# Optimization experiments

Hardware: AMD Instinct MI355X
Metric: run time of the kernel (lower is better)

## Reference

```python
import jax, jax.numpy as jnp
from jax import lax
import numpy as np

# pywt Wavelet('db4') decomposition filters
DEC_LO = jnp.array([-0.010597401784997278, 0.032883011666982945, 0.030841381835986965,
                    -0.18703481171888114, -0.027983769416983848, 0.6308807679295904,
                    0.7148465705525415, 0.23037781330885523], dtype=jnp.float32)
DEC_HI = jnp.array([-0.23037781330885523, 0.7148465705525415, -0.6308807679295904,
                    -0.027983769416983848, 0.18703481171888114, 0.030841381835986965,
                    -0.032883011666982945, -0.010597401784997278], dtype=jnp.float32)
FLT = 8
BN_INV = np.float32(1.0 / np.sqrt(1.0 + 1e-5))  # BatchNorm eval: running_mean=0, running_var=1


def dwt_db4(v):
    """Vectorized pywt.dwt(v, 'db4', mode='symmetric') along the last axis.
    v: (..., n) -> (cA, cD), each (..., (n+FLT-1)//2).
    pywt: symmetric-pad by FLT-1, true convolution with filter, take valid[1::2].
    Equivalent: correlate padded[1:...] with flipped filter, stride 2."""
    n = v.shape[-1]
    out_len = (n + FLT - 1) // 2
    xp = jnp.pad(v, [(0, 0)] * (v.ndim - 1) + [(FLT - 1, FLT - 1)], mode='symmetric')
    xp = xp[..., 1:1 + 2 * (out_len - 1) + FLT]
    lead = v.shape[:-1]
    xr = xp.reshape(-1, 1, xp.shape[-1])                      # (N*, 1, L)
    kern = jnp.stack([DEC_LO[::-1], DEC_HI[::-1]])[:, None, :]  # (2, 1, 8)
    y = lax.conv_general_dilated(xr, kern, (2,), 'VALID',
                                 dimension_numbers=('NCH', 'OIH', 'NCH'))
    return y[:, 0].reshape(lead + (out_len,)), y[:, 1].reshape(lead + (out_len,))


def conv_bn_relu(x, w, g, b):
    # x: (B, C, S); w: (O, I, K) no bias; BN in eval mode; ReLU; dropout off (eval)
    k = w.shape[-1]
    p = (k - 1) // 2
    y = lax.conv_general_dilated(x, w, (1,), [(p, p)],
                                 dimension_numbers=('NCH', 'OIH', 'NCH'))
    return jax.nn.relu((g * BN_INV)[None, :, None] * y + b[None, :, None])


def setup_inputs() -> dict:
    key = jax.random.key(0)
    ks = jax.random.split(key, 16)
    C, S, B = 88, 2048, 4
    d = dict()
    d['x'] = jax.random.normal(ks[0], (B, S, C), dtype=jnp.float32)
    d['w1'] = jax.random.normal(ks[1], (C, C, 1), dtype=jnp.float32) * 0.05
    d['w2a'] = jax.random.normal(ks[2], (C, C, 1), dtype=jnp.float32) * 0.05
    d['w2b'] = jax.random.normal(ks[3], (C, C, 3), dtype=jnp.float32) * 0.05
    d['w3a'] = jax.random.normal(ks[4], (C, C, 1), dtype=jnp.float32) * 0.05
    d['w3b'] = jax.random.normal(ks[5], (C, C, 3), dtype=jnp.float32) * 0.05
    d['w3c'] = jax.random.normal(ks[6], (C, C, 5), dtype=jnp.float32) * 0.05
    for nm in ['g1', 'g2a', 'g2b', 'g3a', 'g3b', 'g3c']:
        d[nm] = jnp.ones((C,), dtype=jnp.float32)
    for nm in ['b1', 'b2a', 'b2b', 'b3a', 'b3b', 'b3c']:
        d[nm] = jnp.zeros((C,), dtype=jnp.float32)
    d['Wmp'] = jax.random.normal(ks[7], (C, 3 * C), dtype=jnp.float32) * 0.05
    d['bmp'] = jnp.zeros((C,), dtype=jnp.float32)
    d['Wq'] = jax.random.normal(ks[8], (C, C), dtype=jnp.float32) * 0.1
    d['Wk'] = jax.random.normal(ks[9], (C, C), dtype=jnp.float32) * 0.1
    d['Wv'] = jax.random.normal(ks[10], (C, C), dtype=jnp.float32) * 0.1
    d['Wout'] = jax.random.normal(ks[11], (C, 112), dtype=jnp.float32) * 0.05
    d['bout'] = jnp.zeros((C,), dtype=jnp.float32)
    return d


def reference(x, w1, g1, b1, w2a, g2a, b2a, w2b, g2b, b2b,
              w3a, g3a, b3a, w3b, g3b, b3b, w3c, g3c, b3c,
              Wmp, bmp, Wq, Wk, Wv, Wout, bout):
    B, S, H = x.shape
    head = 4
    dk = H // head                                # 22
    wd = dk // 2 + 3 if dk % 2 == 0 else (dk + 1) // 2 + 3  # 14
    xt = jnp.swapaxes(x, 1, 2)                    # (B, C, S)
    # mutil_Parallel: three conv lines + fuse + residual
    x1 = conv_bn_relu(xt, w1, g1, b1)
    x2 = conv_bn_relu(conv_bn_relu(xt, w2a, g2a, b2a), w2b, g2b, b2b)
    x3 = conv_bn_relu(conv_bn_relu(conv_bn_relu(xt, w3a, g3a, b3a), w3b, g3b, b3b), w3c, g3c, b3c)
    cat = jnp.concatenate([x1, x2, x3], axis=1)   # (B, 3C, S)
    mp = jnp.einsum('bcs,oc->bso', cat, Wmp) + bmp + x  # (B, S, C)
    identity = mp
    # multi-head attention with wavelet-transformed values
    scale = dk ** (-0.5)
    q = jnp.einsum('bsh,oh->bso', mp, Wq).reshape(B, S, head, dk).transpose(0, 2, 1, 3) * scale
    k = jnp.einsum('bsh,oh->bso', mp, Wk).reshape(B, S, head, dk).transpose(0, 2, 1, 3)
    v = jnp.einsum('bsh,oh->bso', mp, Wv).reshape(B, S, head, dk).transpose(0, 2, 1, 3)
    attn = jax.nn.softmax(jnp.einsum('bhqd,bhkd->bhqk', q, k), axis=-1)  # (B,4,S,S)
    cA, cD = dwt_db4(v)                           # each (B, 4, S, 14)
    wcd = jnp.einsum('bhqk,bhkd->bhqd', attn, cD)  # (B, 4, S, 14)
    xo = jax.nn.relu(wcd.transpose(0, 2, 1, 3).reshape(B, S, head * wd))
    cAr = cA.reshape(B, S, head * wd)             # faithful to source's direct .view
    out = jnp.concatenate([xo, cAr], axis=-1) @ Wout.T + bout
    return identity + out
```

## Files before the change

### kernel.cpp

```cpp
#include <hip/hip_runtime.h>

#define BN_INV  0.99999500003749981f
#define QSCALE  0.21320071635561041f

typedef unsigned int uint;
typedef unsigned short u16;
typedef __attribute__((ext_vector_type(8))) short s16x8;
typedef __attribute__((ext_vector_type(4))) float f32x4;

#define OFF_BCAT 0
#define OFF_V    512
#define OFF_MP   721408
#define SW0    2884608
#define SB1    (SW0)
#define SB2B   (SW0+30720)
#define SB3B   (SW0+67584)
#define SB3C   (SW0+104448)
#define SBMP   (SW0+165888)
#define SBQKV  (SW0+202752)
#define SBOUT  (SW0+239616)
#define SXB    3148800
#define SXCAT  3869696
#define SX2    6032384
#define ST3B   6753280
#define SX3    7474176
#define SMPB   8195072
#define SQB    3869696
#define SKB    4918272
#define SCDT   5966848
#define SXOB   6753280

__constant__ float c_dlo[8] = {-0.010597401784997278f, 0.032883011666982945f,
    0.030841381835986965f, -0.18703481171888114f, -0.02798376941698385f,
    0.6308807679295904f, 0.7148465705525415f, 0.23037781330885523f};
__constant__ float c_dhi[8] = {-0.23037781330885523f, 0.7148465705525415f,
    -0.6308807679295904f, -0.02798376941698385f, 0.18703481171888114f,
    0.030841381835986965f, -0.032883011666982945f, -0.010597401784997278f};

__device__ __forceinline__ u16 f2bf(float f) {
    uint u = __float_as_uint(f);
    uint r = u + 0x7fffu + ((u >> 16) & 1u);
    return (u16)(r >> 16);
}

__global__ __launch_bounds__(256) void prepk(
    const float* __restrict__ x,
    const float* __restrict__ w1, const float* __restrict__ w2a, const float* __restrict__ w2b,
    const float* __restrict__ w3a, const float* __restrict__ w3b, const float* __restrict__ w3c,
    const float* __restrict__ g1, const float* __restrict__ g2a, const float* __restrict__ g2b,
    const float* __restrict__ g3a, const float* __restrict__ g3b, const float* __restrict__ g3c,
    const float* __restrict__ b1, const float* __restrict__ b2a, const float* __restrict__ b3a,
    const float* __restrict__ Wmp, const float* __restrict__ Wq, const float* __restrict__ Wk,
    const float* __restrict__ Wv, const float* __restrict__ Wout, float* __restrict__ ws)
{
    u16* wu = (u16*)ws;
    int r = blockIdx.x * 256 + threadIdx.x;
    if (r < 264) {
        ws[OFF_BCAT + r] = (r < 88) ? b1[r] : (r < 176 ? b2a[r-88] : b3a[r-176]);
        return;
    }
    r -= 264;
    if (r < 320*96) {
        int n = r / 96, kk = r % 96; float v = 0.f;
        if (kk < 88 && n < 264) {
            if (n < 88)       v = w1 [n*88+kk]       * g1 [n];
            else if (n < 176) v = w2a[(n-88)*88+kk]  * g2a[n-88];
            else              v = w3a[(n-176)*88+kk] * g3a[n-176];
            v *= BN_INV;
        }
        wu[SB1 + r] = f2bf(v); return;
    }
    r -= 320*96;
    if (r < 128*288) {
        int n = r / 288, kk = r % 288, t = kk/96, i = kk%96; float v = 0.f;
        if (n < 88 && i < 88) v = w2b[n*264 + i*3 + t] * g2b[n] * BN_INV;
        wu[SB2B + r] = f2bf(v); return;
    }
    r -= 128*288;
    if (r < 128*288) {
        int n = r / 288, kk = r % 288, t = kk/96, i = kk%96; float v = 0.f;
        if (n < 88 && i < 88) v = w3b[n*264 + i*3 + t] * g3b[n] * BN_INV;
        wu[SB3B + r] = f2bf(v); return;
    }
    r -= 128*288;
    if (r < 128*480) {
        int n = r / 480, kk = r % 480, t = kk/96, i = kk%96; float v = 0.f;
        if (n < 88 && i < 88) v = w3c[n*440 + i*5 + t] * g3c[n] * BN_INV;
        wu[SB3C + r] = f2bf(v); return;
    }
    r -= 128*480;
    if (r < 128*288) {
        int n = r / 288, kk = r % 288, c = kk/96, i = kk%96; float v = 0.f;
        if (n < 88 && i < 88) v = Wmp[n*264 + c*88 + i];
        wu[SBMP + r] = f2bf(v); return;
    }
    r -= 128*288;
    if (r < 384*96) {
        int n = r / 96, kk = r % 96, sec = n / 128, o = n % 128; float v = 0.f;
        if (o < 88 && kk < 88) {
            if (sec == 0)      v = Wq[o*88+kk] * QSCALE;
            else if (sec == 1) v = Wk[o*88+kk];
            else               v = Wv[o*88+kk];
        }
        wu[SBQKV + r] = f2bf(v); return;
    }
    r -= 384*96;
    if (r < 128*192) {
        int n = r / 192, kk = r % 192; float v = 0.f;
        if (n < 88 && kk < 112) v = Wout[n*112 + kk];
        wu[SBOUT + r] = f2bf(v); return;
    }
    r -= 128*192;
    if (r < 8192*88) {
        wu[SXB + r] = f2bf(x[r]); return;
    }
}

struct GemmChunks {
    int soff[5];
    int stride[5];
    int cols[5];
};

template<int NCH, int HALO, int MODE, int OUTM>
__global__ __launch_bounds__(256) void gemmk(GemmChunks ch,
    const u16* __restrict__ wsrc,
    const u16* __restrict__ Bw, const u16* __restrict__ Bw2,
    const float* __restrict__ bias, const float* __restrict__ bias2,
    const float* __restrict__ resid, int relu,
    u16* __restrict__ outb, u16* __restrict__ outb2,
    float* __restrict__ outf, int outStride, int N)
{
    constexpr int RA   = HALO ? (64 + NCH - 1) : 64 * NCH;
    constexpr int BSTR = NCH * 96 + 8;
    constexpr int KTOT = NCH * 96;
    __shared__ u16 As[RA * 104];
    __shared__ u16 Bs[64 * BSTR];
    int tid = threadIdx.x;
    int lane = tid & 63, w = tid >> 6, wr = w >> 1, wc = w & 1;
    int p0 = blockIdx.x * 64;
    int nb = blockIdx.y;
    int which = (MODE == 2) ? (nb >> 1) : 0;
    int nbl   = (MODE == 2) ? (nb & 1) : nb;
    const u16* Bw_ = (MODE == 2 && which) ? Bw2 : Bw;
    int bs = p0 & ~2047, be = bs + 2048;

    if (HALO) {
        constexpr int OFS = (NCH - 1) / 2;
        int soff = ch.soff[0] + which * 88;
        int stride = ch.stride[0], cols = ch.cols[0];
        for (int e = tid; e < RA * 12; e += 256) {
            int r = e / 12, seg = e % 12;
            int row = p0 + r - OFS;
            int4 v = {0,0,0,0};
            if (row >= bs && row < be && seg*8 < cols)
                v = *(const int4*)&wsrc[(size_t)soff + (size_t)row*stride + seg*8];
            *(int4*)&As[r*104 + seg*8] = v;
        }
    } else {
        for (int e = tid; e < NCH * 768; e += 256) {
            int c = e / 768, rem = e - c*768;
            int r = rem / 12, seg = rem % 12;
            int row = p0 + r;
            int4 v = {0,0,0,0};
            if (seg*8 < ch.cols[c])
                v = *(const int4*)&wsrc[(size_t)ch.soff[c] + (size_t)row*ch.stride[c] + seg*8];
            *(int4*)&As[c*6656 + r*104 + seg*8] = v;
        }
    }
    for (int e = tid; e < 64 * NCH * 12; e += 256) {
        int n = e / (NCH*12), seg = e % (NCH*12);
        *(int4*)&Bs[n*BSTR + seg*8] =
            *(const int4*)&Bw_[((size_t)(nbl*64 + n))*KTOT + seg*8];
    }
    __syncthreads();

    f32x4 acc[2][2];
    #pragma unroll
    for (int a = 0; a < 2; a++)
        #pragma unroll
        for (int b = 0; b < 2; b++) acc[a][b] = (f32x4){0.f,0.f,0.f,0.f};

    int ar0 = (wr*32 + (lane&15))*104 + (lane>>4)*8;
    int br0 = (wc*32 + (lane&15))*BSTR + (lane>>4)*8;

    #pragma unroll
    for (int c = 0; c < NCH; c++) {
        int abase = HALO ? (ar0 + c*104) : (c*6656 + ar0);
        int bbase = br0 + c*96;
        #pragma unroll
        for (int ks = 0; ks < 3; ks++) {
            s16x8 a0 = *(const s16x8*)&As[abase + ks*32];
            s16x8 a1 = *(const s16x8*)&As[abase + 16*104 + ks*32];
            s16x8 b0 = *(const s16x8*)&Bs[bbase + ks*32];
            s16x8 b1 = *(const s16x8*)&Bs[bbase + 16*BSTR + ks*32];
            acc[0][0] = __builtin_amdgcn_mfma_f32_16x16x32_bf16(a0, b0, acc[0][0], 0, 0, 0);
            acc[0][1] = __builtin_amdgcn_mfma_f32_16x16x32_bf16(a0, b1, acc[0][1], 0, 0, 0);
            acc[1][0] = __builtin_amdgcn_mfma_f32_16x16x32_bf16(a1, b0, acc[1][0], 0, 0, 0);
            acc[1][1] = __builtin_amdgcn_mfma_f32_16x16x32_bf16(a1, b1, acc[1][1], 0, 0, 0);
        }
    }

    int rbase = p0 + wr*32 + (lane>>4)*4;
    if (MODE != 1) {
        u16* outb_ = (MODE == 2 && which) ? outb2 : outb;
        const float* bias_ = (MODE == 2 && which) ? bias2 : bias;
        int cbase = nbl*64 + wc*32 + (lane&15);
        #pragma unroll
        for (int fn = 0; fn < 2; fn++) {
            int col = cbase + fn*16;
            if (col < N) {
                float bb = bias_ ? bias_[col] : 0.f;
                #pragma unroll
                for (int fm = 0; fm < 2; fm++)
                    #pragma unroll
                    for (int j = 0; j < 4; j++) {
                        int row = rbase + fm*16 + j;
                        float v = acc[fm][fn][j] + bb;
                        if (relu) v = fmaxf(v, 0.f);
                        if (resid) v += resid[(size_t)row*outStride + col];
                        if (OUTM & 1) outb_[(size_t)row*outStride + col] = f2bf(v);
                        if (OUTM & 2) outf[(size_t)row*outStride + col] = v;
                    }
            }
        }
    } else {
        u16* wq = outb;
        int sec = nb >> 1;
        #pragma unroll
        for (int fn = 0; fn < 2; fn++) {
            int cw = (nb&1)*64 + wc*32 + fn*16 + (lane&15);
            if (cw < 88) {
                int h = cw / 22, d = cw % 22;
                #pragma unroll
                for (int fm = 0; fm < 2; fm++)
                    #pragma unroll
                    for (int j = 0; j < 4; j++) {
                        int row = rbase + fm*16 + j;
                        int b = row >> 11, s = row & 2047;
                        float v = acc[fm][fn][j];
                        if (sec == 0)
                            wq[SQB + ((size_t)(b*4+h)*2048 + s)*32 + d] = f2bf(v);
                        else if (sec == 1)
                            wq[SKB + ((size_t)(b*4+h)*2048 + s)*32 + d] = f2bf(v);
                        else
                            outf[OFF_V + (size_t)row*88 + cw] = v;
                    }
            } else if (sec < 2 && cw < 128) {
                int t = cw - 88, h = t / 10, dpad = 22 + t % 10;
                size_t sqk = (sec == 0) ? (size_t)SQB : (size_t)SKB;
                #pragma unroll
                for (int fm = 0; fm < 2; fm++)
                    #pragma unroll
                    for (int j = 0; j < 4; j++) {
                        int row = rbase + fm*16 + j;
                        int b = row >> 11, s = row & 2047;
                        wq[sqk + ((size_t)(b*4+h)*2048 + s)*32 + dpad] = 0;
                    }
            }
        }
    }
}

__global__ __launch_bounds__(256) void dwtk(float* __restrict__ ws)
{
    u16* wu = (u16*)ws;
    __shared__ float vs[32*89];
    int tid = threadIdx.x;
    int p0 = blockIdx.x * 32;
    const float* V = ws + OFF_V;
    for (int e = tid; e < 32*88; e += 256) {
        int p = e / 88, c = e - p*88;
        vs[p*89 + c] = V[(size_t)p0*88 + e];
    }
    __syncthreads();
    int b = p0 >> 11, sbase = p0 & 2047;
    #pragma unroll
    for (int it = 0; it < 7; it++) {
        int idx = it*256 + tid;
        int p = idx & 31, hjj = idx >> 5;
        int h = hjj / 14, jj = hjj - h*14;
        const float* v = &vs[p*89 + h*22];
        float ca = 0.f, cd = 0.f;
        #pragma unroll
        for (int t = 0; t < 8; t++) {
            int pp = 1 + 2*jj + t;
            int oi = pp < 7 ? 6 - pp : (pp < 29 ? pp - 7 : 50 - pp);
            float vv = v[oi];
            ca = fmaf(vv, c_dlo[7-t], ca);
            cd = fmaf(vv, c_dhi[7-t], cd);
        }
        int s = sbase + p;
        wu[SCDT + ((size_t)((b*4+h)*16 + jj))*2048 + s] = f2bf(cd);
        int hs = h*2048 + s, s2 = hs >> 2, qd = hs & 3;
        wu[SXOB + ((size_t)b*2048 + s2)*112 + 56 + qd*14 + jj] = f2bf(ca);
    }
    {
        int p = tid & 31, t = tid >> 5;
        int h = t >> 1, dd = 14 + (t & 1);
        wu[SCDT + ((size_t)((b*4+h)*16 + dd))*2048 + sbase + p] = 0;
    }
}

__global__ __launch_bounds__(512, 4) void attnk(float* __restrict__ ws)
{
    const u16* wu = (const u16*)ws;
    u16* wua = (u16*)ws;
    __shared__ __align__(16) u16 Kt[2*64*40];
    __shared__ __align__(16) u16 CDt[2*16*72];
    __shared__ __align__(16) u16 Pb[8][16*72];
    int tid = threadIdx.x, lane = tid & 63, w = tid >> 6;
    int bh = blockIdx.y;
    int qsub = w & 3, half = w >> 2;
    int q0 = blockIdx.x * 64 + qsub * 16;
    int qrow = lane & 15, grp = lane >> 4;

    s16x8 qf = *(const s16x8*)&wu[SQB + ((size_t)bh*2048 + q0 + qrow)*32 + grp*8];
    const u16* Kbase = wu + SKB + (size_t)bh*2048*32;
    const u16* Cbase = wu + SCDT + (size_t)bh*16*2048;
    const u16* Kh = &Kt[half*2560];
    const u16* Ch = &CDt[half*1152];

    int khh = tid >> 8, krr = (tid >> 2) & 63, kseg = tid & 3;
    int chh = tid >> 7, cdd = (tid >> 3) & 15, cseg = tid & 7;

    f32x4 o = (f32x4){0.f,0.f,0.f,0.f};
    float m = -1e30f, l = 0.f;

    int4 kreg = *(const int4*)&Kbase[(size_t)(khh*1024 + krr)*32 + kseg*8];
    int4 creg = {0,0,0,0};
    if (tid < 256)
        creg = *(const int4*)&Cbase[(size_t)cdd*2048 + chh*1024 + cseg*8];

    for (int kt = 0; kt < 16; kt++) {
        __syncthreads();
        *(int4*)&Kt[khh*2560 + krr*40 + kseg*8] = kreg;
        if (tid < 256) *(int4*)&CDt[chh*1152 + cdd*72 + cseg*8] = creg;
        __syncthreads();
        if (kt < 15) {
            kreg = *(const int4*)&Kbase[(size_t)(khh*1024 + (kt+1)*64 + krr)*32 + kseg*8];
            if (tid < 256)
                creg = *(const int4*)&Cbase[(size_t)cdd*2048 + chh*1024 + (kt+1)*64 + cseg*8];
        }

        f32x4 s4[4];
        #pragma unroll
        for (int sub = 0; sub < 4; sub++) {
            s16x8 kf = *(const s16x8*)&Kh[(sub*16 + qrow)*40 + grp*8];
            s4[sub] = __builtin_amdgcn_mfma_f32_16x16x32_bf16(kf, qf,
                        (f32x4){0.f,0.f,0.f,0.f}, 0, 0, 0);
        }
        float sv[16];
        #pragma unroll
        for (int sub = 0; sub < 4; sub++)
            #pragma unroll
            for (int j = 0; j < 4; j++) sv[sub*4+j] = s4[sub][j];

        float mx[8];
        #pragma unroll
        for (int i = 0; i < 8; i++) mx[i] = fmaxf(sv[i], sv[i+8]);
        #pragma unroll
        for (int i = 0; i < 4; i++) mx[i] = fmaxf(mx[i], mx[i+4]);
        float tm = fmaxf(fmaxf(mx[0], mx[1]), fmaxf(mx[2], mx[3]));
        tm = fmaxf(tm, __shfl_xor(tm, 16));
        tm = fmaxf(tm, __shfl_xor(tm, 32));

        if (!__all(tm <= m + 8.f)) {
            float mn = fmaxf(m, tm);
            float corr = __expf(m - mn);
            m = mn; l *= corr;
            #pragma unroll
            for (int j = 0; j < 4; j++) o[j] *= __shfl(corr, grp*4 + j);
        }

        float pv[16];
        #pragma unroll
        for (int i = 0; i < 16; i++) pv[i] = __expf(sv[i] - m);
        float sm[8];
        #pragma unroll
        for (int i = 0; i < 8; i++) sm[i] = pv[i] + pv[i+8];
        #pragma unroll
        for (int i = 0; i < 4; i++) sm[i] += sm[i+4];
        float ls = (sm[0] + sm[1]) + (sm[2] + sm[3]);
        ls += __shfl_xor(ls, 16);
        ls += __shfl_xor(ls, 32);
        l += ls;

        {
            uint* pb32 = (uint*)Pb[w];
            #pragma unroll
            for (int sub = 0; sub < 4; sub++) {
                uint u01 = (uint)f2bf(pv[sub*4+0]) | ((uint)f2bf(pv[sub*4+1]) << 16);
                uint u23 = (uint)f2bf(pv[sub*4+2]) | ((uint)f2bf(pv[sub*4+3]) << 16);
                int sa = qrow*72 + sub*16 + grp*4;
                *(uint2*)&pb32[sa >> 1] = make_uint2(u01, u23);
            }
        }
        #pragma unroll
        for (int ks = 0; ks < 2; ks++) {
            s16x8 pa = *(const s16x8*)&Pb[w][qrow*72 + ks*32 + grp*8];
            s16x8 cf = *(const s16x8*)&Ch[qrow*72 + ks*32 + grp*8];
            o = __builtin_amdgcn_mfma_f32_16x16x32_bf16(pa, cf, o, 0, 0, 0);
        }
    }

    __syncthreads();
    float* part = (float*)Kt;
    if (lane < 16) { part[(w*16+lane)*18 + 0] = m; part[(w*16+lane)*18 + 1] = l; }
    #pragma unroll
    for (int j = 0; j < 4; j++) part[(w*16 + grp*4 + j)*18 + 2 + qrow] = o[j];
    __syncthreads();
    if (w < 4) {
        int q = qrow;
        const float* pa = &part[(w*16 + q)*18];
        const float* pb = &part[((w+4)*16 + q)*18];
        float m0 = pa[0], l0 = pa[1], m1 = pb[0], l1 = pb[1];
        float M = fmaxf(m0, m1);
        float e0 = __expf(m0 - M), e1 = __expf(m1 - M);
        float inv = 1.f / (l0*e0 + l1*e1);
        int b = bh >> 2, h = bh & 3;
        int s = blockIdx.x * 64 + w * 16 + q;
        #pragma unroll
        for (int dd = 0; dd < 4; dd++) {
            int d = grp*4 + dd;
            if (d < 14) {
                float val = (pa[2+d]*e0 + pb[2+d]*e1) * inv;
                wua[SXOB + ((size_t)b*2048 + s)*112 + h*14 + d] = f2bf(fmaxf(val, 0.f));
            }
        }
    }
}

extern "C" void kernel_launch(void* const* d_in, const int* in_sizes, int n_in,
                              void* d_out, int out_size, void* d_ws, size_t ws_size,
                              hipStream_t stream) {
    const float* x    = (const float*)d_in[0];
    const float* w1   = (const float*)d_in[1];
    const float* w2a  = (const float*)d_in[2];
    const float* w2b  = (const float*)d_in[3];
    const float* w3a  = (const float*)d_in[4];
    const float* w3b  = (const float*)d_in[5];
    const float* w3c  = (const float*)d_in[6];
    const float* g1   = (const float*)d_in[7];
    const float* g2a  = (const float*)d_in[8];
    const float* g2b  = (const float*)d_in[9];
    const float* g3a  = (const float*)d_in[10];
    const float* g3b  = (const float*)d_in[11];
    const float* g3c  = (const float*)d_in[12];
    const float* b1   = (const float*)d_in[13];
    const float* b2a  = (const float*)d_in[14];
    const float* b2b  = (const float*)d_in[15];
    const float* b3a  = (const float*)d_in[16];
    const float* b3b  = (const float*)d_in[17];
    const float* b3c  = (const float*)d_in[18];
    const float* Wmp  = (const float*)d_in[19];
    const float* bmp  = (const float*)d_in[20];
    const float* Wq   = (const float*)d_in[21];
    const float* Wk   = (const float*)d_in[22];
    const float* Wv   = (const float*)d_in[23];
    const float* Wout = (const float*)d_in[24];
    const float* bout = (const float*)d_in[25];
    float* ws = (float*)d_ws;
    float* out = (float*)d_out;
    u16* wu = (u16*)d_ws;

    prepk<<<3850, 256, 0, stream>>>(x, w1, w2a, w2b, w3a, w3b, w3c,
                                    g1, g2a, g2b, g3a, g3b, g3c,
                                    b1, b2a, b3a, Wmp, Wq, Wk, Wv, Wout, ws);

    {
        GemmChunks c{}; c.soff[0]=SXB; c.stride[0]=88; c.cols[0]=88;
        gemmk<1,1,0,1><<<dim3(128,5), 256, 0, stream>>>(c, wu, wu+SB1, nullptr,
            ws+OFF_BCAT, nullptr, nullptr, 1, wu+SXCAT, nullptr, nullptr, 264, 264);
    }
    {
        GemmChunks c{}; c.soff[0]=SXCAT+88; c.stride[0]=264; c.cols[0]=88;
        gemmk<3,1,2,1><<<dim3(128,4), 256, 0, stream>>>(c, wu, wu+SB2B, wu+SB3B,
            b2b, b3b, nullptr, 1, wu+SX2, wu+ST3B, nullptr, 88, 88);
    }
    {
        GemmChunks c{}; c.soff[0]=ST3B; c.stride[0]=88; c.cols[0]=88;
        gemmk<5,1,0,1><<<dim3(128,2), 256, 0, stream>>>(c, wu, wu+SB3C, nullptr,
            b3c, nullptr, nullptr, 1, wu+SX3, nullptr, nullptr, 88, 88);
    }
    {
        GemmChunks c{};
        c.soff[0]=SXCAT; c.stride[0]=264; c.cols[0]=88;
        c.soff[1]=SX2;   c.stride[1]=88;  c.cols[1]=88;
        c.soff[2]=SX3;   c.stride[2]=88;  c.cols[2]=88;
        gemmk<3,0,0,3><<<dim3(128,2), 256, 0, stream>>>(c, wu, wu+SBMP, nullptr,
            bmp, nullptr, x, 0, wu+SMPB, nullptr, ws+OFF_MP, 88, 88);
    }
    {
        GemmChunks c{}; c.soff[0]=SMPB; c.stride[0]=88; c.cols[0]=88;
        gemmk<1,1,1,0><<<dim3(128,6), 256, 0, stream>>>(c, wu, wu+SBQKV, nullptr,
            nullptr, nullptr, nullptr, 0, wu, nullptr, ws, 0, 0);
    }
    dwtk<<<256, 256, 0, stream>>>(ws);
    attnk<<<dim3(32, 16), 512, 0, stream>>>(ws);
    {
        GemmChunks c{};
        c.soff[0]=SXOB;    c.stride[0]=112; c.cols[0]=96;
        c.soff[1]=SXOB+96; c.stride[1]=112; c.cols[1]=16;
        gemmk<2,0,0,2><<<dim3(128,2), 256, 0, stream>>>(c, wu, wu+SBOUT, nullptr,
            bout, nullptr, ws+OFF_MP, 0, nullptr, nullptr, out, 88, 88);
    }
}
```

Baseline: 197.3 us.

## Fuse conv branches, projection, QKV and DWT into one halo-tiled kernel

Six launches (three conv GEMM stages, the mixing projection, the QKV projection and the DWT) become one kernel. Each block handles 32 rows plus a 3-row halo and keeps every intermediate activation in shared memory, so the bf16 intermediates no longer round-trip through global memory. V stays in LDS and feeds the DWT directly instead of being written as fp32. The cost is only 256 blocks with serialized stages and syncthreads barriers, halo recomputation, B-operand weights read straight from global memory, and heavy LDS use that limits occupancy.

New measurement: 189.1 us. -4.2%, faster.

```diff
diff --git a/kernel.cpp b/kernel.cpp
--- a/kernel.cpp
+++ b/kernel.cpp
@@ -9,7 +9,6 @@
 typedef __attribute__((ext_vector_type(4))) float f32x4;
 
 #define OFF_BCAT 0
-#define OFF_V    512
 #define OFF_MP   721408
 #define SW0    2884608
 #define SB1    (SW0)
@@ -20,11 +19,6 @@
 #define SBQKV  (SW0+202752)
 #define SBOUT  (SW0+239616)
 #define SXB    3148800
-#define SXCAT  3869696
-#define SX2    6032384
-#define ST3B   6753280
-#define SX3    7474176
-#define SMPB   8195072
 #define SQB    3869696
 #define SKB    4918272
 #define SCDT   5966848
@@ -41,6 +35,9 @@
     uint u = __float_as_uint(f);
     uint r = u + 0x7fffu + ((u >> 16) & 1u);
     return (u16)(r >> 16);
+}
+__device__ __forceinline__ float bf2f(u16 u) {
+    return __uint_as_float((uint)u << 16);
 }
 
 __global__ __launch_bounds__(256) void prepk(
@@ -116,62 +113,256 @@
     }
 }
 
+__global__ __launch_bounds__(256) void megak(const float* __restrict__ x,
+    const float* __restrict__ b2b, const float* __restrict__ b3b,
+    const float* __restrict__ b3c, const float* __restrict__ bmp,
+    float* __restrict__ ws)
+{
+    u16* wu = (u16*)ws;
+    __shared__ __align__(16) u16 XBs[48*104];
+    __shared__ __align__(16) u16 TC [52*272];
+    __shared__ __align__(16) u16 T3Bs[36*104];
+    __shared__ __align__(16) u16 X3s[32*104];
+    __shared__ __align__(16) u16 MPBs[32*104];
+    __shared__ __align__(16) u16 Vs[32*96];
+    u16* X2s = XBs;
+
+    int tid = threadIdx.x, lane = tid & 63, w = tid >> 6;
+    int p0 = blockIdx.x * 32;
+    int bs = p0 & ~2047, be = bs + 2048;
+    int qrow = lane & 15, grp = lane >> 4;
+    int rj = grp * 4;
+
+    for (int e = tid; e < 576; e += 256) {
+        int r = e / 12, seg = e % 12;
+        int grow = p0 - 3 + r;
+        int4 v = {0,0,0,0};
+        if (seg < 11 && grow >= 0 && grow < 8192)
+            v = *(const int4*)&wu[SXB + (size_t)grow*88 + seg*8];
+        *(int4*)&XBs[r*104 + seg*8] = v;
+    }
+    __syncthreads();
+
+    for (int p = w; p < 51; p += 4) {
+        int rt = p % 3, ct = p / 3;
+        f32x4 acc = (f32x4){0.f,0.f,0.f,0.f};
+        #pragma unroll
+        for (int ks = 0; ks < 3; ks++) {
+            s16x8 a = *(const s16x8*)&XBs[(rt*16+qrow)*104 + ks*32 + grp*8];
+            s16x8 b = *(const s16x8*)&wu[SB1 + (size_t)(ct*16+qrow)*96 + ks*32 + grp*8];
+            acc = __builtin_amdgcn_mfma_f32_16x16x32_bf16(a, b, acc, 0, 0, 0);
+        }
+        int col = ct*16 + qrow;
+        float bb = (col < 264) ? ws[OFF_BCAT + col] : 0.f;
+        #pragma unroll
+        for (int j = 0; j < 4; j++) {
+            int r = rt*16 + rj + j;
+            int grow = p0 - 3 + r;
+            float v = fmaxf(acc[j] + bb, 0.f);
+            TC[r*272 + col] = (grow >= bs && grow < be) ? f2bf(v) : (u16)0;
+        }
+    }
+    __syncthreads();
+
+    for (int p = w; p < 30; p += 4) {
+        if (p < 12) {
+            int rt = p % 2, ct = p / 2;
+            f32x4 acc = (f32x4){0.f,0.f,0.f,0.f};
+            #pragma unroll
+            for (int t = 0; t < 3; t++)
+                #pragma unroll
+                for (int ks = 0; ks < 3; ks++) {
+                    s16x8 a = *(const s16x8*)&TC[((2+t) + rt*16+qrow)*272 + 88 + ks*32 + grp*8];
+                    s16x8 b = *(const s16x8*)&wu[SB2B + (size_t)(ct*16+qrow)*288 + t*96 + ks*32 + grp*8];
+                    acc = __builtin_amdgcn_mfma_f32_16x16x32_bf16(a, b, acc, 0, 0, 0);
+                }
+            int col = ct*16 + qrow;
+            float bb = (col < 88) ? b2b[col] : 0.f;
+            #pragma unroll
+            for (int j = 0; j < 4; j++) {
+                int i = rt*16 + rj + j;
+                X2s[i*104 + col] = f2bf(fmaxf(acc[j] + bb, 0.f));
+            }
+        } else {
+            int pp = p - 12, rt = pp % 3, ct = pp / 3;
+            f32x4 acc = (f32x4){0.f,0.f,0.f,0.f};
+            #pragma unroll
+            for (int t = 0; t < 3; t++)
+                #pragma unroll
+                for (int ks = 0; ks < 3; ks++) {
+                    s16x8 a = *(const s16x8*)&TC[(rt*16+qrow + t)*272 + 176 + ks*32 + grp*8];
+                    s16x8 b = *(const s16x8*)&wu[SB3B + (size_t)(ct*16+qrow)*288 + t*96 + ks*32 + grp*8];
+                    acc = __builtin_amdgcn_mfma_f32_16x16x32_bf16(a, b, acc, 0, 0, 0);
+                }
+            int col = ct*16 + qrow;
+            float bb = (col < 88) ? b3b[col] : 0.f;
+            #pragma unroll
+            for (int j = 0; j < 4; j++) {
+                int i = rt*16 + rj + j;
+                if (i < 36) {
+                    int grow = p0 - 2 + i;
+                    float v = fmaxf(acc[j] + bb, 0.f);
+                    T3Bs[i*104 + col] = (grow >= bs && grow < be) ? f2bf(v) : (u16)0;
+                }
+            }
+        }
+    }
+    __syncthreads();
+
+    for (int p = w; p < 12; p += 4) {
+        int rt = p % 2, ct = p / 2;
+        f32x4 acc = (f32x4){0.f,0.f,0.f,0.f};
+        #pragma unroll
+        for (int t = 0; t < 5; t++)
+            #pragma unroll
+            for (int ks = 0; ks < 3; ks++) {
+                s16x8 a = *(const s16x8*)&T3Bs[(rt*16+qrow + t)*104 + ks*32 + grp*8];
+                s16x8 b = *(const s16x8*)&wu[SB3C + (size_t)(ct*16+qrow)*480 + t*96 + ks*32 + grp*8];
+                acc = __builtin_amdgcn_mfma_f32_16x16x32_bf16(a, b, acc, 0, 0, 0);
+            }
+        int col = ct*16 + qrow;
+        float bb = (col < 88) ? b3c[col] : 0.f;
+        #pragma unroll
+        for (int j = 0; j < 4; j++) {
+            int i = rt*16 + rj + j;
+            X3s[i*104 + col] = f2bf(fmaxf(acc[j] + bb, 0.f));
+        }
+    }
+    __syncthreads();
+
+    for (int p = w; p < 12; p += 4) {
+        int rt = p % 2, ct = p / 2;
+        f32x4 acc = (f32x4){0.f,0.f,0.f,0.f};
+        #pragma unroll
+        for (int ks = 0; ks < 3; ks++) {
+            s16x8 a = *(const s16x8*)&TC[(3 + rt*16+qrow)*272 + ks*32 + grp*8];
+            s16x8 b = *(const s16x8*)&wu[SBMP + (size_t)(ct*16+qrow)*288 + ks*32 + grp*8];
+            acc = __builtin_amdgcn_mfma_f32_16x16x32_bf16(a, b, acc, 0, 0, 0);
+        }
+        #pragma unroll
+        for (int ks = 0; ks < 3; ks++) {
+            s16x8 a = *(const s16x8*)&X2s[(rt*16+qrow)*104 + ks*32 + grp*8];
+            s16x8 b = *(const s16x8*)&wu[SBMP + (size_t)(ct*16+qrow)*288 + 96 + ks*32 + grp*8];
+            acc = __builtin_amdgcn_mfma_f32_16x16x32_bf16(a, b, acc, 0, 0, 0);
+        }
+        #pragma unroll
+        for (int ks = 0; ks < 3; ks++) {
+            s16x8 a = *(const s16x8*)&X3s[(rt*16+qrow)*104 + ks*32 + grp*8];
+            s16x8 b = *(const s16x8*)&wu[SBMP + (size_t)(ct*16+qrow)*288 + 192 + ks*32 + grp*8];
+            acc = __builtin_amdgcn_mfma_f32_16x16x32_bf16(a, b, acc, 0, 0, 0);
+        }
+        int col = ct*16 + qrow;
+        float bb = (col < 88) ? bmp[col] : 0.f;
+        #pragma unroll
+        for (int j = 0; j < 4; j++) {
+            int i = rt*16 + rj + j;
+            float v = acc[j] + bb;
+            if (col < 88) {
+                v += x[(size_t)(p0+i)*88 + col];
+                ws[OFF_MP + (size_t)(p0+i)*88 + col] = v;
+            } else v = 0.f;
+            MPBs[i*104 + col] = f2bf(v);
+        }
+    }
+    __syncthreads();
+
+    for (int p = w; p < 36; p += 4) {
+        int rt = p % 2, tt = p / 2;
+        int sec = tt / 6, nn = tt % 6;
+        int n0 = sec*128 + nn*16;
+        f32x4 acc = (f32x4){0.f,0.f,0.f,0.f};
+        #pragma unroll
+        for (int ks = 0; ks < 3; ks++) {
+            s16x8 a = *(const s16x8*)&MPBs[(rt*16+qrow)*104 + ks*32 + grp*8];
+            s16x8 b = *(const s16x8*)&wu[SBQKV + (size_t)(n0+qrow)*96 + ks*32 + grp*8];
+            acc = __builtin_amdgcn_mfma_f32_16x16x32_bf16(a, b, acc, 0, 0, 0);
+        }
+        int o = nn*16 + qrow;
+        if (o < 88) {
+            int h = o / 22, d = o % 22;
+            #pragma unroll
+            for (int j = 0; j < 4; j++) {
+                int i = rt*16 + rj + j;
+                int g = p0 + i, b_ = g >> 11, ss = g & 2047;
+                if (sec == 0)
+                    wu[SQB + ((size_t)(b_*4+h)*2048 + ss)*32 + d] = f2bf(acc[j]);
+                else if (sec == 1)
+                    wu[SKB + ((size_t)(b_*4+h)*2048 + ss)*32 + d] = f2bf(acc[j]);
+                else
+                    Vs[i*96 + o] = f2bf(acc[j]);
+            }
+        }
+    }
+    for (int e = tid; e < 2560; e += 256) {
+        int pp = e & 31, r = e >> 5;
+        int arr = r / 40, rr = r % 40, h = rr / 10, dpad = 22 + rr % 10;
+        int g = p0 + pp, b_ = g >> 11, ss = g & 2047;
+        wu[(arr ? SKB : SQB) + ((size_t)(b_*4+h)*2048 + ss)*32 + dpad] = 0;
+    }
+    __syncthreads();
+
+    int b_ = p0 >> 11, sbase = p0 & 2047;
+    #pragma unroll
+    for (int it = 0; it < 7; it++) {
+        int idx = it*256 + tid;
+        int pp = idx & 31, hjj = idx >> 5;
+        int h = hjj / 14, jj = hjj - h*14;
+        const u16* v = &Vs[pp*96 + h*22];
+        float ca = 0.f, cd = 0.f;
+        #pragma unroll
+        for (int t = 0; t < 8; t++) {
+            int q = 1 + 2*jj + t;
+            int oi = q < 7 ? 6 - q : (q < 29 ? q - 7 : 50 - q);
+            float vv = bf2f(v[oi]);
+            ca = fmaf(vv, c_dlo[7-t], ca);
+            cd = fmaf(vv, c_dhi[7-t], cd);
+        }
+        int s = sbase + pp;
+        wu[SCDT + ((size_t)((b_*4+h)*16 + jj))*2048 + s] = f2bf(cd);
+        int hs = h*2048 + s, s2 = hs >> 2, qd = hs & 3;
+        wu[SXOB + ((size_t)b_*2048 + s2)*112 + 56 + qd*14 + jj] = f2bf(ca);
+    }
+    {
+        int pp = tid & 31, t = tid >> 5;
+        int h = t >> 1, dd = 14 + (t & 1);
+        wu[SCDT + ((size_t)((b_*4+h)*16 + dd))*2048 + sbase + pp] = 0;
+    }
+}
+
 struct GemmChunks {
     int soff[5];
     int stride[5];
     int cols[5];
 };
 
-template<int NCH, int HALO, int MODE, int OUTM>
+template<int NCH>
 __global__ __launch_bounds__(256) void gemmk(GemmChunks ch,
-    const u16* __restrict__ wsrc,
-    const u16* __restrict__ Bw, const u16* __restrict__ Bw2,
-    const float* __restrict__ bias, const float* __restrict__ bias2,
-    const float* __restrict__ resid, int relu,
-    u16* __restrict__ outb, u16* __restrict__ outb2,
+    const u16* __restrict__ wsrc, const u16* __restrict__ Bw,
+    const float* __restrict__ bias, const float* __restrict__ resid,
     float* __restrict__ outf, int outStride, int N)
 {
-    constexpr int RA   = HALO ? (64 + NCH - 1) : 64 * NCH;
     constexpr int BSTR = NCH * 96 + 8;
     constexpr int KTOT = NCH * 96;
-    __shared__ u16 As[RA * 104];
+    __shared__ u16 As[64 * NCH * 104];
     __shared__ u16 Bs[64 * BSTR];
     int tid = threadIdx.x;
     int lane = tid & 63, w = tid >> 6, wr = w >> 1, wc = w & 1;
     int p0 = blockIdx.x * 64;
     int nb = blockIdx.y;
-    int which = (MODE == 2) ? (nb >> 1) : 0;
-    int nbl   = (MODE == 2) ? (nb & 1) : nb;
-    const u16* Bw_ = (MODE == 2 && which) ? Bw2 : Bw;
-    int bs = p0 & ~2047, be = bs + 2048;
-
-    if (HALO) {
-        constexpr int OFS = (NCH - 1) / 2;
-        int soff = ch.soff[0] + which * 88;
-        int stride = ch.stride[0], cols = ch.cols[0];
-        for (int e = tid; e < RA * 12; e += 256) {
-            int r = e / 12, seg = e % 12;
-            int row = p0 + r - OFS;
-            int4 v = {0,0,0,0};
-            if (row >= bs && row < be && seg*8 < cols)
-                v = *(const int4*)&wsrc[(size_t)soff + (size_t)row*stride + seg*8];
-            *(int4*)&As[r*104 + seg*8] = v;
-        }
-    } else {
-        for (int e = tid; e < NCH * 768; e += 256) {
-            int c = e / 768, rem = e - c*768;
-            int r = rem / 12, seg = rem % 12;
-            int row = p0 + r;
-            int4 v = {0,0,0,0};
-            if (seg*8 < ch.cols[c])
-                v = *(const int4*)&wsrc[(size_t)ch.soff[c] + (size_t)row*ch.stride[c] + seg*8];
-            *(int4*)&As[c*6656 + r*104 + seg*8] = v;
-        }
+
+    for (int e = tid; e < NCH * 768; e += 256) {
+        int c = e / 768, rem = e - c*768;
+        int r = rem / 12, seg = rem % 12;
+        int row = p0 + r;
+        int4 v = {0,0,0,0};
+        if (seg*8 < ch.cols[c])
+            v = *(const int4*)&wsrc[(size_t)ch.soff[c] + (size_t)row*ch.stride[c] + seg*8];
+        *(int4*)&As[c*6656 + r*104 + seg*8] = v;
     }
     for (int e = tid; e < 64 * NCH * 12; e += 256) {
         int n = e / (NCH*12), seg = e % (NCH*12);
         *(int4*)&Bs[n*BSTR + seg*8] =
-            *(const int4*)&Bw_[((size_t)(nbl*64 + n))*KTOT + seg*8];
+            *(const int4*)&Bw[((size_t)(nb*64 + n))*KTOT + seg*8];
     }
     __syncthreads();
 
@@ -186,7 +377,7 @@
 
     #pragma unroll
     for (int c = 0; c < NCH; c++) {
-        int abase = HALO ? (ar0 + c*104) : (c*6656 + ar0);
+        int abase = c*6656 + ar0;
         int bbase = br0 + c*96;
         #pragma unroll
         for (int ks = 0; ks < 3; ks++) {
@@ -202,103 +393,21 @@
     }
 
     int rbase = p0 + wr*32 + (lane>>4)*4;
-    if (MODE != 1) {
-        u16* outb_ = (MODE == 2 && which) ? outb2 : outb;
-        const float* bias_ = (MODE == 2 && which) ? bias2 : bias;
-        int cbase = nbl*64 + wc*32 + (lane&15);
-        #pragma unroll
-        for (int fn = 0; fn < 2; fn++) {
-            int col = cbase + fn*16;
-            if (col < N) {
-                float bb = bias_ ? bias_[col] : 0.f;
+    int cbase = nb*64 + wc*32 + (lane&15);
+    #pragma unroll
+    for (int fn = 0; fn < 2; fn++) {
+        int col = cbase + fn*16;
+        if (col < N) {
+            float bb = bias[col];
+            #pragma unroll
+            for (int fm = 0; fm < 2; fm++)
                 #pragma unroll
-                for (int fm = 0; fm < 2; fm++)
-                    #pragma unroll
-                    for (int j = 0; j < 4; j++) {
-                        int row = rbase + fm*16 + j;
-                        float v = acc[fm][fn][j] + bb;
-                        if (relu) v = fmaxf(v, 0.f);
-                        if (resid) v += resid[(size_t)row*outStride + col];
-                        if (OUTM & 1) outb_[(size_t)row*outStride + col] = f2bf(v);
-                        if (OUTM & 2) outf[(size_t)row*outStride + col] = v;
-                    }
-            }
-        }
-    } else {
-        u16* wq = outb;
-        int sec = nb >> 1;
-        #pragma unroll
-        for (int fn = 0; fn < 2; fn++) {
-            int cw = (nb&1)*64 + wc*32 + fn*16 + (lane&15);
-            if (cw < 88) {
-                int h = cw / 22, d = cw % 22;
-                #pragma unroll
-                for (int fm = 0; fm < 2; fm++)
-                    #pragma unroll
-                    for (int j = 0; j < 4; j++) {
-                        int row = rbase + fm*16 + j;
-                        int b = row >> 11, s = row & 2047;
-                        float v = acc[fm][fn][j];
-                        if (sec == 0)
-                            wq[SQB + ((size_t)(b*4+h)*2048 + s)*32 + d] = f2bf(v);
-                        else if (sec == 1)
-                            wq[SKB + ((size_t)(b*4+h)*2048 + s)*32 + d] = f2bf(v);
-                        else
-                            outf[OFF_V + (size_t)row*88 + cw] = v;
-                    }
-            } else if (sec < 2 && cw < 128) {
-                int t = cw - 88, h = t / 10, dpad = 22 + t % 10;
-                size_t sqk = (sec == 0) ? (size_t)SQB : (size_t)SKB;
-                #pragma unroll
-                for (int fm = 0; fm < 2; fm++)
-                    #pragma unroll
-                    for (int j = 0; j < 4; j++) {
-                        int row = rbase + fm*16 + j;
-                        int b = row >> 11, s = row & 2047;
-                        wq[sqk + ((size_t)(b*4+h)*2048 + s)*32 + dpad] = 0;
-                    }
-            }
-        }
-    }
-}
-
-__global__ __launch_bounds__(256) void dwtk(float* __restrict__ ws)
-{
-    u16* wu = (u16*)ws;
-    __shared__ float vs[32*89];
-    int tid = threadIdx.x;
-    int p0 = blockIdx.x * 32;
-    const float* V = ws + OFF_V;
-    for (int e = tid; e < 32*88; e += 256) {
-        int p = e / 88, c = e - p*88;
-        vs[p*89 + c] = V[(size_t)p0*88 + e];
-    }
-    __syncthreads();
-    int b = p0 >> 11, sbase = p0 & 2047;
-    #pragma unroll
-    for (int it = 0; it < 7; it++) {
-        int idx = it*256 + tid;
-        int p = idx & 31, hjj = idx >> 5;
-        int h = hjj / 14, jj = hjj - h*14;
-        const float* v = &vs[p*89 + h*22];
-        float ca = 0.f, cd = 0.f;
-        #pragma unroll
-        for (int t = 0; t < 8; t++) {
-            int pp = 1 + 2*jj + t;
-            int oi = pp < 7 ? 6 - pp : (pp < 29 ? pp - 7 : 50 - pp);
-            float vv = v[oi];
-            ca = fmaf(vv, c_dlo[7-t], ca);
-            cd = fmaf(vv, c_dhi[7-t], cd);
-        }
-        int s = sbase + p;
-        wu[SCDT + ((size_t)((b*4+h)*16 + jj))*2048 + s] = f2bf(cd);
-        int hs = h*2048 + s, s2 = hs >> 2, qd = hs & 3;
-        wu[SXOB + ((size_t)b*2048 + s2)*112 + 56 + qd*14 + jj] = f2bf(ca);
-    }
-    {
-        int p = tid & 31, t = tid >> 5;
-        int h = t >> 1, dd = 14 + (t & 1);
-        wu[SCDT + ((size_t)((b*4+h)*16 + dd))*2048 + sbase + p] = 0;
+                for (int j = 0; j < 4; j++) {
+                    int row = rbase + fm*16 + j;
+                    float v = acc[fm][fn][j] + bb + resid[(size_t)row*outStride + col];
+                    outf[(size_t)row*outStride + col] = v;
+                }
+        }
     }
 }
 
@@ -467,42 +576,13 @@
     prepk<<<3850, 256, 0, stream>>>(x, w1, w2a, w2b, w3a, w3b, w3c,
                                     g1, g2a, g2b, g3a, g3b, g3c,
                                     b1, b2a, b3a, Wmp, Wq, Wk, Wv, Wout, ws);
-
-    {
-        GemmChunks c{}; c.soff[0]=SXB; c.stride[0]=88; c.cols[0]=88;
-        gemmk<1,1,0,1><<<dim3(128,5), 256, 0, stream>>>(c, wu, wu+SB1, nullptr,
-            ws+OFF_BCAT, nullptr, nullptr, 1, wu+SXCAT, nullptr, nullptr, 264, 264);
-    }
-    {
-        GemmChunks c{}; c.soff[0]=SXCAT+88; c.stride[0]=264; c.cols[0]=88;
-        gemmk<3,1,2,1><<<dim3(128,4), 256, 0, stream>>>(c, wu, wu+SB2B, wu+SB3B,
-            b2b, b3b, nullptr, 1, wu+SX2, wu+ST3B, nullptr, 88, 88);
-    }
-    {
-        GemmChunks c{}; c.soff[0]=ST3B; c.stride[0]=88; c.cols[0]=88;
-        gemmk<5,1,0,1><<<dim3(128,2), 256, 0, stream>>>(c, wu, wu+SB3C, nullptr,
-            b3c, nullptr, nullptr, 1, wu+SX3, nullptr, nullptr, 88, 88);
-    }
-    {
-        GemmChunks c{};
-        c.soff[0]=SXCAT; c.stride[0]=264; c.cols[0]=88;
-        c.soff[1]=SX2;   c.stride[1]=88;  c.cols[1]=88;
-        c.soff[2]=SX3;   c.stride[2]=88;  c.cols[2]=88;
-        gemmk<3,0,0,3><<<dim3(128,2), 256, 0, stream>>>(c, wu, wu+SBMP, nullptr,
-            bmp, nullptr, x, 0, wu+SMPB, nullptr, ws+OFF_MP, 88, 88);
-    }
-    {
-        GemmChunks c{}; c.soff[0]=SMPB; c.stride[0]=88; c.cols[0]=88;
-        gemmk<1,1,1,0><<<dim3(128,6), 256, 0, stream>>>(c, wu, wu+SBQKV, nullptr,
-            nullptr, nullptr, nullptr, 0, wu, nullptr, ws, 0, 0);
-    }
-    dwtk<<<256, 256, 0, stream>>>(ws);
+    megak<<<256, 256, 0, stream>>>(x, b2b, b3b, b3c, bmp, ws);
     attnk<<<dim3(32, 16), 512, 0, stream>>>(ws);
     {
         GemmChunks c{};
         c.soff[0]=SXOB;    c.stride[0]=112; c.cols[0]=96;
         c.soff[1]=SXOB+96; c.stride[1]=112; c.cols[1]=16;
-        gemmk<2,0,0,2><<<dim3(128,2), 256, 0, stream>>>(c, wu, wu+SBOUT, nullptr,
-            bout, nullptr, ws+OFF_MP, 0, nullptr, nullptr, out, 88, 88);
-    }
-}
+        gemmk<2><<<dim3(128,2), 256, 0, stream>>>(c, wu, wu+SBOUT,
+            bout, ws+OFF_MP, out, 88, 88);
+    }
+}
```
